# Optimization experiments

Hardware: AMD Instinct MI355X
Metric: run time of the kernel (lower is better)

The kernel has to match this reference:

```python
import jax, jax.numpy as jnp
import numpy as np

# ---- static configuration (mirrors repo globals) ----
D_MODEL = 1024   # d_model
B = 128          # batch size
T = 256          # structure sequence length (tgt)
T_C = 128        # max constraints per scene (tgt_c rows)
N_PER = 64       # real (non-padded) constraints per scene
S = 128          # number of source objects per scene (src_e rows)
N_TYPES = 4      # len(constraint_types)
N_DIR = 4        # len(direction_types)
C_TOKEN = 2      # structure_vocab_map['c']
N_C = N_PER * B  # total constraints across the batch (static!)


def setup_inputs() -> dict:
    key = jax.random.key(0)
    ks = jax.random.split(key, 12)
    decoded_output = jax.random.normal(ks[0], (T, B, D_MODEL), jnp.float32)
    # tgt: the first N_PER timesteps of every batch element are constraint tokens 'c'.
    tgt = jnp.where(jnp.arange(T)[:, None] < N_PER, C_TOKEN, 0) * jnp.ones((1, B), jnp.int32)
    tgt = tgt.astype(jnp.int32)
    # tgt_c padding: rows >= N_PER are padding -> exactly N_PER*B = N_C real constraints,
    # laid out row-major (timestep-major, batch-fastest) when flattened.
    tgt_c_padding_mask = jnp.broadcast_to(jnp.arange(T_C)[:, None] >= N_PER, (T_C, B))
    types_col = jax.random.randint(ks[1], (T_C, B), 0, N_TYPES)
    q_col = jax.random.randint(ks[2], (T_C, B), 0, S)
    r_col = jax.random.randint(ks[3], (T_C, B), 0, S)
    tgt_c = jnp.stack([types_col, q_col, r_col], axis=-1).astype(jnp.int32)  # [T_C,B,3]
    src_e = jax.random.normal(ks[4], (S, B, D_MODEL), jnp.float32)
    src_padding_mask = jax.random.uniform(ks[5], (B, S)) < 0.1
    scale = 0.02
    params = {
        'type_emb': jax.random.normal(ks[6], (N_TYPES, D_MODEL), jnp.float32),
        'W_ctype': jax.random.normal(ks[7], (N_TYPES, D_MODEL), jnp.float32) * scale,
        'b_ctype': jnp.zeros((N_TYPES,), jnp.float32),
        'W_obj': jax.random.normal(ks[8], (D_MODEL, 3 * D_MODEL), jnp.float32) * scale,
        'b_obj': jnp.zeros((D_MODEL,), jnp.float32),
        'W_dir': jax.random.normal(ks[9], (N_DIR, 4 * D_MODEL), jnp.float32) * scale,
        'b_dir': jnp.zeros((N_DIR,), jnp.float32),
    }
    return dict(decoded_output=decoded_output, tgt=tgt, tgt_c=tgt_c,
                tgt_c_padding_mask=tgt_c_padding_mask, src_e=src_e,
                src_padding_mask=src_padding_mask, **params)


def reference(decoded_output, tgt, tgt_c, tgt_c_padding_mask, src_e, src_padding_mask,
              type_emb, W_ctype, b_ctype, W_obj, b_obj, W_dir, b_dir):
    d = decoded_output.shape[-1]
    # --- static-count boolean selections (setup guarantees exactly N_C True entries) ---
    idx_struct = jnp.nonzero((tgt == C_TOKEN).reshape(-1), size=N_C)[0]
    heads = decoded_output.reshape(-1, d)[idx_struct]                # [N_C, d]
    idx_c = jnp.nonzero((~tgt_c_padding_mask).reshape(-1), size=N_C)[0]

    # constraint type logits
    type_selections = heads @ W_ctype.T + b_ctype                    # [N_C, N_TYPES]

    # constraint type embeddings
    types = type_emb[tgt_c[:, :, 0].reshape(-1)[idx_c]]              # [N_C, d]

    # q_e: gather query-object embeddings (torch.gather along dim 0)
    q_idx = jnp.broadcast_to(tgt_c[:, :, 1:2], (T_C, B, d))
    q_e = jnp.take_along_axis(src_e, q_idx, axis=0).reshape(-1, d)[idx_c]  # [N_C, d]

    obj_in = jnp.concatenate([heads, types, q_e], axis=1)            # [N_C, 3d]
    pointer = obj_in @ W_obj.T + b_obj                               # [N_C, d]

    batch_ref = jnp.broadcast_to(jnp.arange(B), (T_C, B)).reshape(-1)[idx_c]  # [N_C]
    # Setup layout guarantee: flattened constraint order is (t, b) row-major with b
    # fastest, N_PER constraints per batch -> pointer reshapes to [N_PER, B, d] and the
    # original per-item tensordot loop collapses into one batched einsum.
    ptr = pointer.reshape(N_PER, B, d)
    logits = jnp.einsum('tbd,sbd->tbs', ptr, src_e).reshape(N_C, S)  # [N_C, S]
    object_selections = jnp.where(src_padding_mask[batch_ref], -jnp.inf, logits)

    # r_e: gather reference-object embeddings
    r_idx = jnp.broadcast_to(tgt_c[:, :, 2:3], (T_C, B, d))
    r_e = jnp.take_along_axis(src_e, r_idx, axis=0).reshape(-1, d)[idx_c]    # [N_C, d]

    dir_in = jnp.concatenate([obj_in, r_e], axis=1)                  # [N_C, 4d]
    direction_selections = dir_in @ W_dir.T + b_dir                  # [N_C, N_DIR]
    return (type_selections, object_selections, direction_selections)
```

## Files before the change

### kernel.cpp

```cpp
#include <hip/hip_runtime.h>
#include <hip/hip_bf16.h>
#include <math.h>

#define D_MODEL 1024
#define B_SZ    128
#define S_SZ    128
#define N_C     8192
#define K_OBJ   3072
#define K_DIR   4096

#define TS_OFF  0
#define OS_OFF  (N_C * 4)
#define DS_OFF  (OS_OFF + N_C * S_SZ)

#define NEG_BIG (-1.0e30f)

typedef __attribute__((ext_vector_type(8))) int   i32x8;
typedef __attribute__((ext_vector_type(4))) float f32x4;

#define WS_PTR8   0ull
#define WS_DEC8   8388608ull
#define WS_SRCE8  16777216ull
#define WS_WOBJ8  33554432ull
#define WS_TEMB8  36700160ull

#define SCALE_ONE 0x7F7F7F7F

__device__ __forceinline__ uint2 f32x8_to_fp8(float4 a, float4 b) {
    unsigned lo = 0, hi = 0;
    lo = __builtin_amdgcn_cvt_pk_fp8_f32(a.x, a.y, lo, false);
    lo = __builtin_amdgcn_cvt_pk_fp8_f32(a.z, a.w, lo, true);
    hi = __builtin_amdgcn_cvt_pk_fp8_f32(b.x, b.y, hi, false);
    hi = __builtin_amdgcn_cvt_pk_fp8_f32(b.z, b.w, hi, true);
    return make_uint2(lo, hi);
}
__device__ __forceinline__ unsigned char f32_to_fp8(float x) {
    return (unsigned char)(__builtin_amdgcn_cvt_pk_fp8_f32(x, x, 0, false) & 0xFF);
}

typedef __attribute__((address_space(3))) unsigned int lds_u32;
typedef __attribute__((address_space(1))) const unsigned int glb_u32;
__device__ __forceinline__ void dma16(const void* g, void* l) {
    __builtin_amdgcn_global_load_lds((glb_u32*)g, (lds_u32*)l, 16, 0, 0);
}

__global__ __launch_bounds__(256) void cvt_fp8_all(
    const float* __restrict__ decoded, const float* __restrict__ src_e,
    const float* __restrict__ W_obj,   const float* __restrict__ type_emb,
    unsigned char* __restrict__ dec8,  unsigned char* __restrict__ srce8,
    unsigned char* __restrict__ wobj8, unsigned char* __restrict__ temb8)
{
    const int blk = blockIdx.x;
    const float* src; unsigned char* dst; size_t u;
    if (blk < 4096)        { src = decoded;  dst = dec8;  u = (size_t)blk * 256 + threadIdx.x; }
    else if (blk < 12288)  { src = src_e;    dst = srce8; u = (size_t)(blk - 4096) * 256 + threadIdx.x; }
    else if (blk < 13824)  { src = W_obj;    dst = wobj8; u = (size_t)(blk - 12288) * 256 + threadIdx.x; }
    else                   { src = type_emb; dst = temb8; u = (size_t)(blk - 13824) * 256 + threadIdx.x; }
    const float4* s = (const float4*)src + u * 2;
    float4 a = s[0], b = s[1];
    *(uint2*)(dst + u * 8) = f32x8_to_fp8(a, b);
}

__global__ __launch_bounds__(256) void pointer_fp8(
    const unsigned char* __restrict__ dec8,
    const unsigned char* __restrict__ temb8,
    const unsigned char* __restrict__ srce8,
    const unsigned char* __restrict__ wobj8,
    const int*   __restrict__ tgt_c,
    const float* __restrict__ b_obj,
    unsigned char* __restrict__ ptr_out)
{
    __shared__ __align__(32) unsigned char As[128 * 128];
    __shared__ __align__(32) unsigned char Bs[128 * 128];

    const int tid  = threadIdx.x;
    const int m0   = blockIdx.x * 128;
    const int n0   = blockIdx.y * 128;
    const int lane = tid & 63;
    const int wv   = tid >> 6;

    const int srow = wv * 8 + (lane >> 3);
    const int c16  = lane & 7;
    const unsigned char *pA0[4], *pA1[4], *pA2[4], *pB[4];
    #pragma unroll
    for (int ro = 0; ro < 4; ++ro) {
        int r = ro * 32 + srow;
        int g = (c16 ^ ((r & 3) << 1)) * 16;
        int n = m0 + r;
        int tt = tgt_c[n * 3 + 0];
        int qq = tgt_c[n * 3 + 1];
        pA0[ro] = dec8  + (size_t)n * 1024 + g;
        pA1[ro] = temb8 + (size_t)tt * 1024 + g;
        pA2[ro] = srce8 + ((size_t)qq * B_SZ + r) * 1024 + g;
        pB[ro]  = wobj8 + (size_t)(n0 + r) * K_OBJ + g;
    }

    const int wm   = (wv & 1) * 64;
    const int wn   = (wv >> 1) * 64;
    const int fm   = lane & 15;
    const int quad = lane >> 4;

    f32x4 acc[4][4];
    #pragma unroll
    for (int i = 0; i < 4; ++i)
        #pragma unroll
        for (int j = 0; j < 4; ++j)
            acc[i][j] = (f32x4){0.f, 0.f, 0.f, 0.f};

    for (int ks = 0; ks < K_OBJ / 128; ++ks) {
        const int k0   = ks * 128;
        const int reg  = k0 >> 10;
        const int koff = k0 & 1023;
        #pragma unroll
        for (int ro = 0; ro < 4; ++ro) {
            void* la = As + ro * 4096 + wv * 1024;
            if (reg == 0)      dma16(pA0[ro] + koff, la);
            else if (reg == 1) dma16(pA1[ro] + koff, la);
            else               dma16(pA2[ro] + koff, la);
            dma16(pB[ro] + k0, Bs + ro * 4096 + wv * 1024);
        }
        __syncthreads();

        i32x8 af[4], bfr[4];
        #pragma unroll
        for (int i = 0; i < 4; ++i) {
            int ra = wm + i * 16 + fm;
            af[i] = *(const i32x8*)&As[ra * 128 + ((quad ^ (ra & 3)) << 5)];
        }
        #pragma unroll
        for (int j = 0; j < 4; ++j) {
            int rb = wn + j * 16 + fm;
            bfr[j] = *(const i32x8*)&Bs[rb * 128 + ((quad ^ (rb & 3)) << 5)];
        }
        #pragma unroll
        for (int i = 0; i < 4; ++i)
            #pragma unroll
            for (int j = 0; j < 4; ++j)
                acc[i][j] = __builtin_amdgcn_mfma_scale_f32_16x16x128_f8f6f4(
                    af[i], bfr[j], acc[i][j], 0, 0, 0, SCALE_ONE, 0, SCALE_ONE);
        __syncthreads();
    }

    #pragma unroll
    for (int j = 0; j < 4; ++j) {
        int ncol = n0 + wn + j * 16 + fm;
        float bo = b_obj[ncol];
        #pragma unroll
        for (int i = 0; i < 4; ++i) {
            int mrow = m0 + wm + i * 16 + quad * 4;
            f32x4 c = acc[i][j];
            #pragma unroll
            for (int r2 = 0; r2 < 4; ++r2)
                ptr_out[(size_t)(mrow + r2) * D_MODEL + ncol] = f32_to_fp8(c[r2] + bo);
        }
    }
}

__global__ __launch_bounds__(256) void logits_fp8(
    const unsigned char* __restrict__ ptr8,
    const unsigned char* __restrict__ srce8,
    const void*  __restrict__ src_pm,
    float*       __restrict__ out_os)
{
    __shared__ __align__(32) unsigned char As[64 * 128];
    __shared__ __align__(32) unsigned char Bs[64 * 128];
    __shared__ int s_flag;

    const int tid  = threadIdx.x;
    const int b    = blockIdx.x;
    const int s0   = blockIdx.y * 64;
    const int lane = tid & 63;
    const int wv   = tid >> 6;

    if (tid == 0) s_flag = 0;
    __syncthreads();
    {
        const int* pmi = (const int*)src_pm;
        int local = 0;
        for (int i = tid; i < 4096; i += 256) local |= (pmi[i] > 1);
        if (local) atomicOr(&s_flag, 1);
    }

    const int srow = wv * 8 + (lane >> 3);
    const int c16  = lane & 7;
    const unsigned char *pA[2], *pBt[2];
    #pragma unroll
    for (int ro = 0; ro < 2; ++ro) {
        int r = ro * 32 + srow;
        int g = (c16 ^ ((r & 3) << 1)) * 16;
        pA[ro]  = ptr8  + ((size_t)r * B_SZ + b) * 1024 + g;
        pBt[ro] = srce8 + ((size_t)(s0 + r) * B_SZ + b) * 1024 + g;
    }

    const int wm   = (wv & 1) * 32;
    const int wn   = (wv >> 1) * 32;
    const int fm   = lane & 15;
    const int quad = lane >> 4;

    f32x4 acc[2][2];
    #pragma unroll
    for (int i = 0; i < 2; ++i)
        #pragma unroll
        for (int j = 0; j < 2; ++j)
            acc[i][j] = (f32x4){0.f, 0.f, 0.f, 0.f};

    for (int ks = 0; ks < D_MODEL / 128; ++ks) {
        const int k0 = ks * 128;
        #pragma unroll
        for (int ro = 0; ro < 2; ++ro) {
            dma16(pA[ro]  + k0, As + ro * 4096 + wv * 1024);
            dma16(pBt[ro] + k0, Bs + ro * 4096 + wv * 1024);
        }
        __syncthreads();

        i32x8 af[2], bfr[2];
        #pragma unroll
        for (int i = 0; i < 2; ++i) {
            int ra = wm + i * 16 + fm;
            af[i] = *(const i32x8*)&As[ra * 128 + ((quad ^ (ra & 3)) << 5)];
        }
        #pragma unroll
        for (int j = 0; j < 2; ++j) {
            int rb = wn + j * 16 + fm;
            bfr[j] = *(const i32x8*)&Bs[rb * 128 + ((quad ^ (rb & 3)) << 5)];
        }
        #pragma unroll
        for (int i = 0; i < 2; ++i)
            #pragma unroll
            for (int j = 0; j < 2; ++j)
                acc[i][j] = __builtin_amdgcn_mfma_scale_f32_16x16x128_f8f6f4(
                    af[i], bfr[j], acc[i][j], 0, 0, 0, SCALE_ONE, 0, SCALE_ONE);
        __syncthreads();
    }

    const bool u8 = (s_flag != 0);
    const unsigned char* pm8  = (const unsigned char*)src_pm;
    const int*           pm32 = (const int*)src_pm;

    #pragma unroll
    for (int j = 0; j < 2; ++j) {
        int s = s0 + wn + j * 16 + fm;
        bool m = u8 ? (pm8[b * S_SZ + s] != 0) : (pm32[b * S_SZ + s] != 0);
        #pragma unroll
        for (int i = 0; i < 2; ++i) {
            int t = wm + i * 16 + quad * 4;
            f32x4 c = acc[i][j];
            #pragma unroll
            for (int r2 = 0; r2 < 4; ++r2)
                out_os[(size_t)((t + r2) * B_SZ + b) * S_SZ + s] = m ? NEG_BIG : c[r2];
        }
    }
}

__global__ __launch_bounds__(256) void typedir_kernel(
    const float* __restrict__ decoded,
    const int*   __restrict__ tgt_c,
    const float* __restrict__ src_e,
    const float* __restrict__ type_emb,
    const float* __restrict__ W_ctype,
    const float* __restrict__ b_ctype,
    const float* __restrict__ W_dir,
    const float* __restrict__ b_dir,
    float*       __restrict__ out)
{
    const int tid = threadIdx.x;
    const int n0  = blockIdx.x * 4;

    __shared__ int s_idx[4][3];
    if (tid < 12) s_idx[tid / 3][tid % 3] = tgt_c[(n0 + tid / 3) * 3 + (tid % 3)];
    __syncthreads();

    float acct[4][4] = {};
    float accd[4][4] = {};

    #pragma unroll 4
    for (int it = 0; it < 16; ++it) {
        int k      = tid + it * 256;
        int region = k >> 10;
        int koff   = k & 1023;

        float wd0 = W_dir[0 * K_DIR + k];
        float wd1 = W_dir[1 * K_DIR + k];
        float wd2 = W_dir[2 * K_DIR + k];
        float wd3 = W_dir[3 * K_DIR + k];
        float wc0 = 0.f, wc1 = 0.f, wc2 = 0.f, wc3 = 0.f;
        if (region == 0) {
            wc0 = W_ctype[0 * D_MODEL + koff];
            wc1 = W_ctype[1 * D_MODEL + koff];
            wc2 = W_ctype[2 * D_MODEL + koff];
            wc3 = W_ctype[3 * D_MODEL + koff];
        }

        #pragma unroll
        for (int r = 0; r < 4; ++r) {
            int n = n0 + r;
            int b = n & 127;
            float a;
            if (region == 0)      a = decoded[(size_t)n * D_MODEL + koff];
            else if (region == 1) a = type_emb[(size_t)s_idx[r][0] * D_MODEL + koff];
            else if (region == 2) a = src_e[((size_t)s_idx[r][1] * B_SZ + b) * D_MODEL + koff];
            else                  a = src_e[((size_t)s_idx[r][2] * B_SZ + b) * D_MODEL + koff];

            accd[r][0] += a * wd0;
            accd[r][1] += a * wd1;
            accd[r][2] += a * wd2;
            accd[r][3] += a * wd3;
            if (region == 0) {
                acct[r][0] += a * wc0;
                acct[r][1] += a * wc1;
                acct[r][2] += a * wc2;
                acct[r][3] += a * wc3;
            }
        }
    }

    __shared__ float red[4][32];
    const int lane = tid & 63;
    const int wave = tid >> 6;

    float vals[32];
    #pragma unroll
    for (int r = 0; r < 4; ++r)
        #pragma unroll
        for (int c = 0; c < 4; ++c) {
            vals[r * 4 + c]      = acct[r][c];
            vals[16 + r * 4 + c] = accd[r][c];
        }

    #pragma unroll
    for (int x = 0; x < 32; ++x) {
        float v = vals[x];
        #pragma unroll
        for (int off = 32; off > 0; off >>= 1)
            v += __shfl_down(v, off, 64);
        vals[x] = v;
    }
    if (lane == 0)
        #pragma unroll
        for (int x = 0; x < 32; ++x) red[wave][x] = vals[x];
    __syncthreads();

    if (tid < 32) {
        float v = red[0][tid] + red[1][tid] + red[2][tid] + red[3][tid];
        int r = (tid & 15) >> 2;
        int c = tid & 3;
        int n = n0 + r;
        if (tid < 16) out[TS_OFF + (size_t)n * 4 + c] = v + b_ctype[c];
        else          out[DS_OFF + (size_t)n * 4 + c] = v + b_dir[c];
    }
}

extern "C" void kernel_launch(void* const* d_in, const int* in_sizes, int n_in,
                              void* d_out, int out_size, void* d_ws, size_t ws_size,
                              hipStream_t stream) {
    const float* decoded  = (const float*)d_in[0];
    const int*   tgt_c    = (const int*)d_in[2];
    const float* src_e    = (const float*)d_in[4];
    const void*  src_pm   = d_in[5];
    const float* type_emb = (const float*)d_in[6];
    const float* W_ctype  = (const float*)d_in[7];
    const float* b_ctype  = (const float*)d_in[8];
    const float* W_obj    = (const float*)d_in[9];
    const float* b_obj    = (const float*)d_in[10];
    const float* W_dir    = (const float*)d_in[11];
    const float* b_dir    = (const float*)d_in[12];

    float* out = (float*)d_out;
    char*  ws  = (char*)d_ws;
    unsigned char* ptr8  = (unsigned char*)(ws + WS_PTR8);
    unsigned char* dec8  = (unsigned char*)(ws + WS_DEC8);
    unsigned char* srce8 = (unsigned char*)(ws + WS_SRCE8);
    unsigned char* wobj8 = (unsigned char*)(ws + WS_WOBJ8);
    unsigned char* temb8 = (unsigned char*)(ws + WS_TEMB8);

    cvt_fp8_all<<<13826, 256, 0, stream>>>(
        decoded, src_e, W_obj, type_emb, dec8, srce8, wobj8, temb8);

    pointer_fp8<<<dim3(N_C / 128, D_MODEL / 128), 256, 0, stream>>>(
        dec8, temb8, srce8, wobj8, tgt_c, b_obj, ptr8);

    typedir_kernel<<<N_C / 4, 256, 0, stream>>>(
        decoded, tgt_c, src_e, type_emb, W_ctype, b_ctype, W_dir, b_dir, out);

    logits_fp8<<<dim3(B_SZ, 2), 256, 0, stream>>>(
        ptr8, srce8, src_pm, out + OS_OFF);
}
```

Measured before the change: 328.4 us.

## Pre-pack FP8 operands into tiled K-chunk layouts with gather fused into conversion

The conversion kernel now does the type/query-object gather while converting, writing the A operand of the pointer GEMM as a contiguous pre-tiled FP8 buffer. W_obj and src_e are also repacked into 16-byte K-chunk-major tiles. The pointer GEMM writes its output in the chunked layout the logits GEMM reads, so every DMA to LDS becomes a fully coalesced 1 KB block. This removes the per-row scattered gathers and the XOR swizzle, at the cost of a larger conversion pass with more workspace traffic and split 16-byte LDS reads in place of single 32-byte reads.

```diff
diff --git a/kernel.cpp b/kernel.cpp
--- a/kernel.cpp
+++ b/kernel.cpp
@@ -16,13 +16,14 @@
 #define NEG_BIG (-1.0e30f)
 
 typedef __attribute__((ext_vector_type(8))) int   i32x8;
+typedef __attribute__((ext_vector_type(4))) int   i32x4;
 typedef __attribute__((ext_vector_type(4))) float f32x4;
 
-#define WS_PTR8   0ull
-#define WS_DEC8   8388608ull
-#define WS_SRCE8  16777216ull
-#define WS_WOBJ8  33554432ull
-#define WS_TEMB8  36700160ull
+#define WS_A8  0ull
+#define WS_W8  25165824ull
+#define WS_E8  28311552ull
+#define WS_P8  45088768ull
+#define RBSTRIDE 196608
 
 #define SCALE_ONE 0x7F7F7F7F
 
@@ -44,56 +45,77 @@
     __builtin_amdgcn_global_load_lds((glb_u32*)g, (lds_u32*)l, 16, 0, 0);
 }
 
-__global__ __launch_bounds__(256) void cvt_fp8_all(
+__global__ __launch_bounds__(256) void cvt_pack_fp8(
     const float* __restrict__ decoded, const float* __restrict__ src_e,
     const float* __restrict__ W_obj,   const float* __restrict__ type_emb,
-    unsigned char* __restrict__ dec8,  unsigned char* __restrict__ srce8,
-    unsigned char* __restrict__ wobj8, unsigned char* __restrict__ temb8)
+    const int*   __restrict__ tgt_c,
+    unsigned char* __restrict__ A8, unsigned char* __restrict__ E8,
+    unsigned char* __restrict__ W8)
 {
     const int blk = blockIdx.x;
-    const float* src; unsigned char* dst; size_t u;
-    if (blk < 4096)        { src = decoded;  dst = dec8;  u = (size_t)blk * 256 + threadIdx.x; }
-    else if (blk < 12288)  { src = src_e;    dst = srce8; u = (size_t)(blk - 4096) * 256 + threadIdx.x; }
-    else if (blk < 13824)  { src = W_obj;    dst = wobj8; u = (size_t)(blk - 12288) * 256 + threadIdx.x; }
-    else                   { src = type_emb; dst = temb8; u = (size_t)(blk - 13824) * 256 + threadIdx.x; }
-    const float4* s = (const float4*)src + u * 2;
-    float4 a = s[0], b = s[1];
-    *(uint2*)(dst + u * 8) = f32x8_to_fp8(a, b);
+    if (blk < 12288) {
+        size_t u  = (size_t)blk * 256 + threadIdx.x;
+        int rb    = (int)(u / 24576);
+        int rem   = (int)(u % 24576);
+        int kc    = rem >> 7;
+        int rem2  = rem & 127;
+        int r     = rem2 >> 1;
+        int half  = rem2 & 1;
+        int n     = rb * 64 + r;
+        int k     = kc * 16 + half * 8;
+        const float* src;
+        if (k < 1024)       src = decoded  + (size_t)n * 1024 + k;
+        else if (k < 2048)  src = type_emb + (size_t)tgt_c[n * 3 + 0] * 1024 + (k - 1024);
+        else                src = src_e + ((size_t)tgt_c[n * 3 + 1] * B_SZ + (n & 127)) * 1024 + (k - 2048);
+        float4 a = ((const float4*)src)[0];
+        float4 b = ((const float4*)src)[1];
+        *(uint2*)(A8 + u * 8) = f32x8_to_fp8(a, b);
+    } else if (blk < 20480) {
+        size_t u  = (size_t)(blk - 12288) * 256 + threadIdx.x;
+        int b     = (int)(u >> 14);
+        int rem   = (int)(u & 16383);
+        int kc    = rem >> 8;
+        int rem2  = rem & 255;
+        int s     = rem2 >> 1;
+        int half  = rem2 & 1;
+        const float* src = src_e + ((size_t)s * B_SZ + b) * 1024 + kc * 16 + half * 8;
+        float4 a = ((const float4*)src)[0];
+        float4 bb = ((const float4*)src)[1];
+        *(uint2*)(E8 + u * 8) = f32x8_to_fp8(a, bb);
+    } else {
+        size_t u  = (size_t)(blk - 20480) * 256 + threadIdx.x;
+        int rb    = (int)(u / 24576);
+        int rem   = (int)(u % 24576);
+        int kc    = rem >> 7;
+        int rem2  = rem & 127;
+        int r     = rem2 >> 1;
+        int half  = rem2 & 1;
+        int j     = rb * 64 + r;
+        int k     = kc * 16 + half * 8;
+        const float* src = W_obj + (size_t)j * K_OBJ + k;
+        float4 a = ((const float4*)src)[0];
+        float4 b = ((const float4*)src)[1];
+        *(uint2*)(W8 + u * 8) = f32x8_to_fp8(a, b);
+    }
 }
 
 __global__ __launch_bounds__(256) void pointer_fp8(
-    const unsigned char* __restrict__ dec8,
-    const unsigned char* __restrict__ temb8,
-    const unsigned char* __restrict__ srce8,
-    const unsigned char* __restrict__ wobj8,
-    const int*   __restrict__ tgt_c,
+    const unsigned char* __restrict__ A8,
+    const unsigned char* __restrict__ W8,
     const float* __restrict__ b_obj,
-    unsigned char* __restrict__ ptr_out)
+    unsigned char* __restrict__ P8)
 {
-    __shared__ __align__(32) unsigned char As[128 * 128];
-    __shared__ __align__(32) unsigned char Bs[128 * 128];
+    __shared__ __align__(16) unsigned char As[16384];
+    __shared__ __align__(16) unsigned char Bs[16384];
 
     const int tid  = threadIdx.x;
-    const int m0   = blockIdx.x * 128;
-    const int n0   = blockIdx.y * 128;
     const int lane = tid & 63;
     const int wv   = tid >> 6;
-
-    const int srow = wv * 8 + (lane >> 3);
-    const int c16  = lane & 7;
-    const unsigned char *pA0[4], *pA1[4], *pA2[4], *pB[4];
-    #pragma unroll
-    for (int ro = 0; ro < 4; ++ro) {
-        int r = ro * 32 + srow;
-        int g = (c16 ^ ((r & 3) << 1)) * 16;
-        int n = m0 + r;
-        int tt = tgt_c[n * 3 + 0];
-        int qq = tgt_c[n * 3 + 1];
-        pA0[ro] = dec8  + (size_t)n * 1024 + g;
-        pA1[ro] = temb8 + (size_t)tt * 1024 + g;
-        pA2[ro] = srce8 + ((size_t)qq * B_SZ + r) * 1024 + g;
-        pB[ro]  = wobj8 + (size_t)(n0 + r) * K_OBJ + g;
-    }
+    const int bx   = blockIdx.x;
+    const int by   = blockIdx.y;
+
+    const unsigned char* gA = A8 + (size_t)(bx * 2) * RBSTRIDE + (size_t)lane * 16;
+    const unsigned char* gB = W8 + (size_t)(by * 2) * RBSTRIDE + (size_t)lane * 16;
 
     const int wm   = (wv & 1) * 64;
     const int wn   = (wv >> 1) * 64;
@@ -108,16 +130,16 @@
             acc[i][j] = (f32x4){0.f, 0.f, 0.f, 0.f};
 
     for (int ks = 0; ks < K_OBJ / 128; ++ks) {
-        const int k0   = ks * 128;
-        const int reg  = k0 >> 10;
-        const int koff = k0 & 1023;
-        #pragma unroll
-        for (int ro = 0; ro < 4; ++ro) {
-            void* la = As + ro * 4096 + wv * 1024;
-            if (reg == 0)      dma16(pA0[ro] + koff, la);
-            else if (reg == 1) dma16(pA1[ro] + koff, la);
-            else               dma16(pA2[ro] + koff, la);
-            dma16(pB[ro] + k0, Bs + ro * 4096 + wv * 1024);
+        const int kcb = ks * 8;
+        #pragma unroll
+        for (int i = 0; i < 4; ++i) {
+            int unit = i * 4 + wv;
+            int rbL  = unit >> 3;
+            int c    = unit & 7;
+            size_t go = (size_t)rbL * RBSTRIDE + (size_t)(kcb + c) * 1024;
+            int    lo = rbL * 8192 + c * 1024;
+            dma16(gA + go, As + lo);
+            dma16(gB + go, Bs + lo);
         }
         __syncthreads();
 
@@ -125,12 +147,18 @@
         #pragma unroll
         for (int i = 0; i < 4; ++i) {
             int ra = wm + i * 16 + fm;
-            af[i] = *(const i32x8*)&As[ra * 128 + ((quad ^ (ra & 3)) << 5)];
+            int base = (ra >> 6) * 8192 + (ra & 63) * 16;
+            i32x4 lo = *(const i32x4*)&As[base + (2 * quad) * 1024];
+            i32x4 hi = *(const i32x4*)&As[base + (2 * quad + 1) * 1024];
+            af[i] = (i32x8){lo[0], lo[1], lo[2], lo[3], hi[0], hi[1], hi[2], hi[3]};
         }
         #pragma unroll
         for (int j = 0; j < 4; ++j) {
             int rb = wn + j * 16 + fm;
-            bfr[j] = *(const i32x8*)&Bs[rb * 128 + ((quad ^ (rb & 3)) << 5)];
+            int base = (rb >> 6) * 8192 + (rb & 63) * 16;
+            i32x4 lo = *(const i32x4*)&Bs[base + (2 * quad) * 1024];
+            i32x4 hi = *(const i32x4*)&Bs[base + (2 * quad + 1) * 1024];
+            bfr[j] = (i32x8){lo[0], lo[1], lo[2], lo[3], hi[0], hi[1], hi[2], hi[3]};
         }
         #pragma unroll
         for (int i = 0; i < 4; ++i)
@@ -143,27 +171,29 @@
 
     #pragma unroll
     for (int j = 0; j < 4; ++j) {
-        int ncol = n0 + wn + j * 16 + fm;
+        int ncol = by * 128 + wn + j * 16 + fm;
         float bo = b_obj[ncol];
+        size_t kco = (size_t)(ncol >> 4) * 1024 + (size_t)bx * 16 + (ncol & 15);
         #pragma unroll
         for (int i = 0; i < 4; ++i) {
-            int mrow = m0 + wm + i * 16 + quad * 4;
             f32x4 c = acc[i][j];
             #pragma unroll
-            for (int r2 = 0; r2 < 4; ++r2)
-                ptr_out[(size_t)(mrow + r2) * D_MODEL + ncol] = f32_to_fp8(c[r2] + bo);
+            for (int r2 = 0; r2 < 4; ++r2) {
+                int b = wm + i * 16 + quad * 4 + r2;
+                P8[(size_t)b * 65536 + kco] = f32_to_fp8(c[r2] + bo);
+            }
         }
     }
 }
 
 __global__ __launch_bounds__(256) void logits_fp8(
-    const unsigned char* __restrict__ ptr8,
-    const unsigned char* __restrict__ srce8,
+    const unsigned char* __restrict__ P8,
+    const unsigned char* __restrict__ E8,
     const void*  __restrict__ src_pm,
     float*       __restrict__ out_os)
 {
-    __shared__ __align__(32) unsigned char As[64 * 128];
-    __shared__ __align__(32) unsigned char Bs[64 * 128];
+    __shared__ __align__(16) unsigned char As[8192];
+    __shared__ __align__(16) unsigned char Bs[8192];
     __shared__ int s_flag;
 
     const int tid  = threadIdx.x;
@@ -181,16 +211,8 @@
         if (local) atomicOr(&s_flag, 1);
     }
 
-    const int srow = wv * 8 + (lane >> 3);
-    const int c16  = lane & 7;
-    const unsigned char *pA[2], *pBt[2];
-    #pragma unroll
-    for (int ro = 0; ro < 2; ++ro) {
-        int r = ro * 32 + srow;
-        int g = (c16 ^ ((r & 3) << 1)) * 16;
-        pA[ro]  = ptr8  + ((size_t)r * B_SZ + b) * 1024 + g;
-        pBt[ro] = srce8 + ((size_t)(s0 + r) * B_SZ + b) * 1024 + g;
-    }
+    const unsigned char* gA = P8 + (size_t)b * 65536  + (size_t)lane * 16;
+    const unsigned char* gB = E8 + (size_t)b * 131072 + (size_t)s0 * 16 + (size_t)lane * 16;
 
     const int wm   = (wv & 1) * 32;
     const int wn   = (wv >> 1) * 32;
@@ -204,12 +226,13 @@
         for (int j = 0; j < 2; ++j)
             acc[i][j] = (f32x4){0.f, 0.f, 0.f, 0.f};
 
-    for (int ks = 0; ks < D_MODEL / 128; ++ks) {
-        const int k0 = ks * 128;
-        #pragma unroll
-        for (int ro = 0; ro < 2; ++ro) {
-            dma16(pA[ro]  + k0, As + ro * 4096 + wv * 1024);
-            dma16(pBt[ro] + k0, Bs + ro * 4096 + wv * 1024);
+    for (int ks = 0; ks < 8; ++ks) {
+        const int kcb = ks * 8;
+        #pragma unroll
+        for (int i = 0; i < 2; ++i) {
+            int c = i * 4 + wv;
+            dma16(gA + (size_t)(kcb + c) * 1024, As + c * 1024);
+            dma16(gB + (size_t)(kcb + c) * 2048, Bs + c * 1024);
         }
         __syncthreads();
 
@@ -217,12 +240,16 @@
         #pragma unroll
         for (int i = 0; i < 2; ++i) {
             int ra = wm + i * 16 + fm;
-            af[i] = *(const i32x8*)&As[ra * 128 + ((quad ^ (ra & 3)) << 5)];
+            i32x4 lo = *(const i32x4*)&As[(2 * quad) * 1024 + ra * 16];
+            i32x4 hi = *(const i32x4*)&As[(2 * quad + 1) * 1024 + ra * 16];
+            af[i] = (i32x8){lo[0], lo[1], lo[2], lo[3], hi[0], hi[1], hi[2], hi[3]};
         }
         #pragma unroll
         for (int j = 0; j < 2; ++j) {
             int rb = wn + j * 16 + fm;
-            bfr[j] = *(const i32x8*)&Bs[rb * 128 + ((quad ^ (rb & 3)) << 5)];
+            i32x4 lo = *(const i32x4*)&Bs[(2 * quad) * 1024 + rb * 16];
+            i32x4 hi = *(const i32x4*)&Bs[(2 * quad + 1) * 1024 + rb * 16];
+            bfr[j] = (i32x8){lo[0], lo[1], lo[2], lo[3], hi[0], hi[1], hi[2], hi[3]};
         }
         #pragma unroll
         for (int i = 0; i < 2; ++i)
@@ -367,21 +394,20 @@
 
     float* out = (float*)d_out;
     char*  ws  = (char*)d_ws;
-    unsigned char* ptr8  = (unsigned char*)(ws + WS_PTR8);
-    unsigned char* dec8  = (unsigned char*)(ws + WS_DEC8);
-    unsigned char* srce8 = (unsigned char*)(ws + WS_SRCE8);
-    unsigned char* wobj8 = (unsigned char*)(ws + WS_WOBJ8);
-    unsigned char* temb8 = (unsigned char*)(ws + WS_TEMB8);
-
-    cvt_fp8_all<<<13826, 256, 0, stream>>>(
-        decoded, src_e, W_obj, type_emb, dec8, srce8, wobj8, temb8);
+    unsigned char* A8 = (unsigned char*)(ws + WS_A8);
+    unsigned char* W8 = (unsigned char*)(ws + WS_W8);
+    unsigned char* E8 = (unsigned char*)(ws + WS_E8);
+    unsigned char* P8 = (unsigned char*)(ws + WS_P8);
+
+    cvt_pack_fp8<<<22016, 256, 0, stream>>>(
+        decoded, src_e, W_obj, type_emb, tgt_c, A8, E8, W8);
 
     pointer_fp8<<<dim3(N_C / 128, D_MODEL / 128), 256, 0, stream>>>(
-        dec8, temb8, srce8, wobj8, tgt_c, b_obj, ptr8);
+        A8, W8, b_obj, P8);
 
     typedir_kernel<<<N_C / 4, 256, 0, stream>>>(
         decoded, tgt_c, src_e, type_emb, W_ctype, b_ctype, W_dir, b_dir, out);
 
     logits_fp8<<<dim3(B_SZ, 2), 256, 0, stream>>>(
-        ptr8, srce8, src_pm, out + OS_OFF);
-}
+        P8, E8, src_pm, out + OS_OFF);
+}
```

Result: slower. 342.8 us (+4.4%).
